# Kernel optimization log

Measured on AMD Instinct MI355X. Metric: run time of the kernel, lower is better.

## Reference

```python
import jax, jax.numpy as jnp
import numpy as np

L2_LAMDA = 0.001
RECONS_LAMDA = 0.2
LB_TH = 0.01
B, N, D = 32, 2048, 256


def setup_inputs() -> dict:
    key = jax.random.key(0)
    k1, k2, k3, k4 = jax.random.split(key, 4)
    cur = jax.random.normal(k1, (B, N, D), jnp.float32)
    pre = jax.random.normal(k2, (B, N, D), jnp.float32)
    lim_r = float(np.sqrt(6.0 / (D + D)))  # xavier_uniform bound
    r_proj = jax.random.uniform(k3, (D, D), jnp.float32, -lim_r, lim_r)
    lim_i = float(np.sqrt(6.0 / (N + N)))
    incidence_m = jax.random.uniform(k4, (N, N), jnp.float32, -lim_i, lim_i)
    return {"cur": cur, "pre": pre, "r_proj": r_proj, "incidence_m": incidence_m}


def reference(cur, pre, r_proj, incidence_m):
    # torch forward detaches cur/pre
    cur = jax.lax.stop_gradient(cur)
    pre = jax.lax.stop_gradient(pre)
    # clamp(min=lb_th) then zero where not (> lb_th)  ==  keep original where > lb_th else 0
    W = jnp.where(incidence_m > LB_TH, incidence_m, 0.0)          # (N, N)
    proj = jnp.einsum('bnd,de->bne', cur, r_proj)                 # (B, N, D)
    neigh = jnp.einsum('nm,bmd->bnd', W, pre)                     # (B, N, D)
    recon_err = jnp.sqrt(jnp.sum((proj - neigh) ** 2, axis=-1))   # (B, N)
    # torch: max(sum(abs(row[None,:]), dim=0)) == max-abs of the masked row
    l1 = jnp.max(jnp.abs(W), axis=1)                              # (N,)
    l2 = jnp.sqrt(jnp.sum(W ** 2, axis=1))                        # (N,)
    per_node = recon_err * RECONS_LAMDA + l1[None, :] + L2_LAMDA * l2[None, :]
    loss = jnp.sum(per_node, axis=1, keepdims=True)               # (B, 1)
    return loss, incidence_m
```

## Files before the change

kernel.cpp:

```cpp
#include <hip/hip_runtime.h>


typedef __attribute__((ext_vector_type(8))) short bf16x8;
typedef __attribute__((ext_vector_type(8))) unsigned short ushort8;
typedef __attribute__((ext_vector_type(16))) float f32x16;

__device__ __forceinline__ unsigned short f2bf(float f) {
    union { float f; unsigned u; } x; x.f = f;
    unsigned r = x.u + 0x7fffu + ((x.u >> 16) & 1u);
    return (unsigned short)(r >> 16);
}

#define GLL16(g, l)                                                         \
    __builtin_amdgcn_global_load_lds(                                       \
        (const __attribute__((address_space(1))) void*)(g),                 \
        (__attribute__((address_space(3))) void*)(l), 16, 0, 0)

__device__ __forceinline__ void transpose_64x64(
    const float* __restrict__ src, unsigned short* __restrict__ dst,
    int R, int C, int r0, int c0, unsigned short* __restrict__ tile) {
    const int t = threadIdx.x;
    const int fr = t >> 4, fc = (t & 15) * 4;
#pragma unroll
    for (int it = 0; it < 4; ++it) {
        int m = fr + it * 16;
        float4 v = *(const float4*)(src + (size_t)(r0 + m) * C + c0 + fc);
        tile[(fc + 0) * 68 + m] = f2bf(v.x);
        tile[(fc + 1) * 68 + m] = f2bf(v.y);
        tile[(fc + 2) * 68 + m] = f2bf(v.z);
        tile[(fc + 3) * 68 + m] = f2bf(v.w);
    }
    __syncthreads();
    const int d = t >> 2, m0 = (t & 3) * 16;
    unsigned short v[16];
#pragma unroll
    for (int j = 0; j < 4; ++j)
        *(ushort4*)(v + j * 4) = *(const ushort4*)(tile + d * 68 + m0 + j * 4);
    unsigned short* dp = dst + (size_t)(c0 + d) * R + r0 + m0;
    ushort8 p0, p1;
#pragma unroll
    for (int j = 0; j < 8; ++j) { p0[j] = v[j]; p1[j] = v[8 + j]; }
    *(ushort8*)(dp) = p0;
    *(ushort8*)(dp + 8) = p1;
}

__global__ __launch_bounds__(256) void prep_all(
    const float* __restrict__ inc, float* __restrict__ out_inc,
    unsigned short* __restrict__ Wneg, float* __restrict__ crow,
    const float* __restrict__ pre, unsigned short* __restrict__ preT,
    const float* __restrict__ r_proj, unsigned short* __restrict__ rprojT) {
    __shared__ unsigned short tile[64 * 68];
    __shared__ float smax[4], ssum[4];
    const int bid = blockIdx.x;
    const int t = threadIdx.x;

    if (bid < 2048) {
        const int row = bid;
        const float4* src = (const float4*)(inc + (size_t)row * 2048);
        float4* dst = (float4*)(out_inc + (size_t)row * 2048);
        ushort4* wp = (ushort4*)(Wneg + (size_t)row * 2048);
        float lmax = 0.f, ss = 0.f;
#pragma unroll
        for (int it = 0; it < 2; ++it) {
            int i = it * 256 + t;
            float4 v = src[i];
            dst[i] = v;
            float w0 = v.x > 0.01f ? v.x : 0.f;
            float w1 = v.y > 0.01f ? v.y : 0.f;
            float w2 = v.z > 0.01f ? v.z : 0.f;
            float w3 = v.w > 0.01f ? v.w : 0.f;
            ushort4 p;
            p.x = f2bf(-w0); p.y = f2bf(-w1); p.z = f2bf(-w2); p.w = f2bf(-w3);
            wp[i] = p;
            lmax = fmaxf(lmax, fmaxf(fmaxf(w0, w1), fmaxf(w2, w3)));
            ss += w0 * w0 + w1 * w1 + w2 * w2 + w3 * w3;
        }
#pragma unroll
        for (int off = 32; off; off >>= 1) {
            lmax = fmaxf(lmax, __shfl_down(lmax, off));
            ss += __shfl_down(ss, off);
        }
        int wv = t >> 6, ln = t & 63;
        if (ln == 0) { smax[wv] = lmax; ssum[wv] = ss; }
        __syncthreads();
        if (t == 0) {
            float m = fmaxf(fmaxf(smax[0], smax[1]), fmaxf(smax[2], smax[3]));
            float s = ssum[0] + ssum[1] + ssum[2] + ssum[3];
            crow[row] = m + 0.001f * sqrtf(s);
        }
    } else if (bid < 6144) {
        const int tt = bid - 2048;
        const int b = tt >> 7;
        const int mt = (tt & 127) >> 2;
        const int dt = tt & 3;
        transpose_64x64(pre + (size_t)b * 524288, preT + (size_t)b * 524288,
                        2048, 256, mt * 64, dt * 64, tile);
    } else {
        const int tt = bid - 6144;
        transpose_64x64(r_proj, rprojT, 256, 256, (tt >> 2) * 64, (tt & 3) * 64,
                        tile);
    }
}

__global__ __launch_bounds__(256, 2) void gemm_diff(
    const unsigned short* __restrict__ Wneg,
    const float* __restrict__ cur,
    const unsigned short* __restrict__ preT,
    const unsigned short* __restrict__ rprojT,
    float* __restrict__ Ssq)
{
    const int n0 = blockIdx.x * 128;
    const int b  = blockIdx.y;

    __shared__ unsigned short Al[128 * 64];
    __shared__ unsigned short Bl[256 * 64];
    __shared__ float ssq[128];

    const int tid  = threadIdx.x;
    const int w    = tid >> 6;
    const int lane = tid & 63;
    const int l32  = lane & 31;
    const int half = lane >> 5;
    const int wm   = w >> 1, wn = w & 1;

    if (tid < 128) ssq[tid] = 0.f;

    f32x16 acc[2][4] = {};

    const float*          curB = cur  + (size_t)b * 2048 * 256;
    const unsigned short* preB = preT + (size_t)b * 256 * 2048;

    const int grow  = lane >> 3;
    const int gbyte = ((lane & 7) ^ grow) * 16;
    const int sw    = (l32 & 7) * 8;

    for (int kt = 0; kt < 36; ++kt) {
        __syncthreads();
        if (kt < 32) {
            const int k0 = kt * 64;
            const unsigned short* ab = Wneg + (size_t)n0 * 2048 + k0;
#pragma unroll
            for (int j = 0; j < 4; ++j) {
                const int row = w * 32 + j * 8 + grow;
                GLL16((const char*)(ab + (size_t)row * 2048) + gbyte,
                      (char*)Al + w * 4096 + j * 1024);
            }
            const unsigned short* bb = preB + k0;
#pragma unroll
            for (int j = 0; j < 8; ++j) {
                const int row = w * 64 + j * 8 + grow;
                GLL16((const char*)(bb + (size_t)row * 2048) + gbyte,
                      (char*)Bl + w * 8192 + j * 1024);
            }
        } else {
            const int kk = kt * 64 - 2048;
            const int r16 = tid >> 4, k4 = tid & 15;
#pragma unroll
            for (int i = 0; i < 8; ++i) {
                const int row = r16 + i * 16;
                float4 v = *(const float4*)(curB + (size_t)(n0 + row) * 256 + kk + k4 * 4);
                ushort4 p;
                p.x = f2bf(v.x); p.y = f2bf(v.y); p.z = f2bf(v.z); p.w = f2bf(v.w);
                const int pos = ((k4 >> 1) ^ (row & 7)) * 8 + (k4 & 1) * 4;
                *(ushort4*)(Al + row * 64 + pos) = p;
            }
            const unsigned short* bb = rprojT + kk;
#pragma unroll
            for (int j = 0; j < 8; ++j) {
                const int row = w * 64 + j * 8 + grow;
                GLL16((const char*)(bb + (size_t)row * 256) + gbyte,
                      (char*)Bl + w * 8192 + j * 1024);
            }
        }
        __syncthreads();

#pragma unroll
        for (int ks = 0; ks < 4; ++ks) {
            const int ck = (ks * 2 + half) * 8;
            bf16x8 af[2], bfr[4];
#pragma unroll
            for (int mi = 0; mi < 2; ++mi)
                af[mi] = *(const bf16x8*)(Al + (wm * 64 + mi * 32 + l32) * 64 +
                                          (ck ^ sw));
#pragma unroll
            for (int ni = 0; ni < 4; ++ni)
                bfr[ni] = *(const bf16x8*)(Bl + (wn * 128 + ni * 32 + l32) * 64 +
                                           (ck ^ sw));
#pragma unroll
            for (int mi = 0; mi < 2; ++mi)
#pragma unroll
                for (int ni = 0; ni < 4; ++ni)
                    acc[mi][ni] = __builtin_amdgcn_mfma_f32_32x32x16_bf16(
                        af[mi], bfr[ni], acc[mi][ni], 0, 0, 0);
        }
    }
    __syncthreads();

#pragma unroll
    for (int mi = 0; mi < 2; ++mi)
#pragma unroll
        for (int reg = 0; reg < 16; ++reg) {
            float s = 0.f;
#pragma unroll
            for (int ni = 0; ni < 4; ++ni) {
                float v = acc[mi][ni][reg];
                s += v * v;
            }
            s += __shfl_xor(s, 1);
            s += __shfl_xor(s, 2);
            s += __shfl_xor(s, 4);
            s += __shfl_xor(s, 8);
            s += __shfl_xor(s, 16);
            if (l32 == 0) {
                const int row = (reg & 3) + 8 * (reg >> 2) + 4 * half;
                atomicAdd(&ssq[wm * 64 + mi * 32 + row], s);
            }
        }
    __syncthreads();
    if (tid < 128)
        Ssq[(size_t)b * 2048 + n0 + tid] = sqrtf(ssq[tid]);
}

__global__ void finalize(const float* __restrict__ Ssq,
                         const float* __restrict__ crow,
                         float* __restrict__ out) {
    const int b = blockIdx.x;
    float s1 = 0.f, s2 = 0.f;
    for (int i = threadIdx.x; i < 2048; i += 256) {
        s1 += Ssq[(size_t)b * 2048 + i];
        s2 += crow[i];
    }
#pragma unroll
    for (int off = 32; off; off >>= 1) {
        s1 += __shfl_down(s1, off);
        s2 += __shfl_down(s2, off);
    }
    __shared__ float sm1[4], sm2[4];
    int wv = threadIdx.x >> 6, ln = threadIdx.x & 63;
    if (ln == 0) { sm1[wv] = s1; sm2[wv] = s2; }
    __syncthreads();
    if (threadIdx.x == 0)
        out[b] = 0.2f * (sm1[0] + sm1[1] + sm1[2] + sm1[3])
               + (sm2[0] + sm2[1] + sm2[2] + sm2[3]);
}

extern "C" void kernel_launch(void* const* d_in, const int* in_sizes, int n_in,
                              void* d_out, int out_size, void* d_ws, size_t ws_size,
                              hipStream_t stream) {
    const float* cur    = (const float*)d_in[0];
    const float* pre    = (const float*)d_in[1];
    const float* r_proj = (const float*)d_in[2];
    const float* inc    = (const float*)d_in[3];
    float* out = (float*)d_out;

    char* ws = (char*)d_ws;
    unsigned short* Wneg   = (unsigned short*)(ws + 0);
    unsigned short* preT   = (unsigned short*)(ws + 8388608);
    unsigned short* rprojT = (unsigned short*)(ws + 41943040);
    float*          Sbuf   = (float*)(ws + 42074112);
    float*          crow   = (float*)(ws + 42336256);

    prep_all<<<6160, 256, 0, stream>>>(inc, out + 32, Wneg, crow,
                                       pre, preT, r_proj, rprojT);
    gemm_diff<<<dim3(16, 32), 256, 0, stream>>>(Wneg, cur, preT, rprojT, Sbuf);
    finalize<<<32, 256, 0, stream>>>(Sbuf, crow, out);
}
```

Before: 248.8 us.

## Enlarge GEMM tile to 256x256 with double-buffered LDS and phased prefetch pipeline

The fused diff GEMM moves from 128x256 tiles with 4 waves to 256x256 tiles with 8 waves (512 threads). The main K loop over W·pre now uses double-buffered LDS with global_load_lds prefetches interleaved across quarter-tile MFMA phases, fine-grained vmcnt waits, barriers and s_setprio around MFMA bursts. The goal is to hide global load latency and halve redundant B-tile traffic per output. In exchange it uses much more LDS (128KB+), which limits occupancy to one block per CU, and the grid shrinks to 256 blocks.

```diff
diff --git a/kernel.cpp b/kernel.cpp
--- a/kernel.cpp
+++ b/kernel.cpp
@@ -102,107 +102,162 @@
     }
 }
 
-__global__ __launch_bounds__(256, 2) void gemm_diff(
+__global__ __launch_bounds__(512, 2) void gemm_diff(
     const unsigned short* __restrict__ Wneg,
     const float* __restrict__ cur,
     const unsigned short* __restrict__ preT,
     const unsigned short* __restrict__ rprojT,
     float* __restrict__ Ssq)
 {
-    const int n0 = blockIdx.x * 128;
+    const int n0 = blockIdx.x * 256;
     const int b  = blockIdx.y;
 
-    __shared__ unsigned short Al[128 * 64];
-    __shared__ unsigned short Bl[256 * 64];
-    __shared__ float ssq[128];
-
-    const int tid  = threadIdx.x;
-    const int w    = tid >> 6;
-    const int lane = tid & 63;
-    const int l32  = lane & 31;
-    const int half = lane >> 5;
-    const int wm   = w >> 1, wn = w & 1;
-
-    if (tid < 128) ssq[tid] = 0.f;
-
-    f32x16 acc[2][4] = {};
-
-    const float*          curB = cur  + (size_t)b * 2048 * 256;
-    const unsigned short* preB = preT + (size_t)b * 256 * 2048;
-
+    __shared__ unsigned short Al[2][256 * 64];
+    __shared__ unsigned short Bl[2][256 * 64];
+    __shared__ float ssq[256];
+
+    const int tid   = threadIdx.x;
+    const int w     = tid >> 6;
+    const int lane  = tid & 63;
+    const int l32   = lane & 31;
+    const int half  = lane >> 5;
+    const int wm128 = (w >> 2) * 128;
+    const int wn64  = (w & 3) * 64;
+    const int w8    = w * 8;
     const int grow  = lane >> 3;
     const int gbyte = ((lane & 7) ^ grow) * 16;
     const int sw    = (l32 & 7) * 8;
 
-    for (int kt = 0; kt < 36; ++kt) {
+    if (tid < 256) ssq[tid] = 0.f;
+
+    f32x16 acc[4][2] = {};
+
+    const float*          curB = cur  + (size_t)b * 2048 * 256;
+    const unsigned short* preB = preT + (size_t)b * 256 * 2048;
+    const unsigned short* An   = Wneg + (size_t)n0 * 2048;
+
+#define STAGE_A(AP, qa, K0)                                                    \
+    {                                                                          \
+        _Pragma("unroll") for (int pass = 0; pass < 2; ++pass) {               \
+            const int rowb = (qa) * 64 + pass * 128 + w8;                      \
+            GLL16((const char*)(An + (size_t)(rowb + grow) * 2048 + (K0)) + gbyte, \
+                  (char*)(AP) + rowb * 128);                                   \
+        }                                                                      \
+    }
+#define STAGE_B(BP, u, K0)                                                     \
+    {                                                                          \
+        _Pragma("unroll") for (int pass = 0; pass < 2; ++pass) {               \
+            const int rowb = (u) * 128 + pass * 64 + w8;                       \
+            GLL16((const char*)(preB + (size_t)(rowb + grow) * 2048 + (K0)) + gbyte, \
+                  (char*)(BP) + rowb * 128);                                   \
+        }                                                                      \
+    }
+
+    STAGE_A(Al[0], 0, 0);
+    STAGE_B(Bl[0], 0, 0);
+    STAGE_B(Bl[0], 1, 0);
+    STAGE_A(Al[0], 1, 0);
+    STAGE_A(Al[1], 0, 64);
+    asm volatile("s_waitcnt vmcnt(2)" ::: "memory");
+    asm volatile("s_barrier" ::: "memory");
+
+    bf16x8 bfr[2][2];
+
+#define LOADB(BP, kh)                                                          \
+    _Pragma("unroll") for (int ni = 0; ni < 2; ++ni)                           \
+    _Pragma("unroll") for (int ksl = 0; ksl < 2; ++ksl)                        \
+        bfr[ni][ksl] = *(const bf16x8*)((BP) + (wn64 + ni * 32 + l32) * 64 +   \
+                           (((((kh) * 2 + ksl) * 2 + half) * 8) ^ sw));
+
+#define PHASE(AP, qa, kh, STAGES, VMW)                                         \
+    {                                                                          \
+        bf16x8 af[2][2];                                                       \
+        _Pragma("unroll") for (int mi = 0; mi < 2; ++mi)                       \
+        _Pragma("unroll") for (int ksl = 0; ksl < 2; ++ksl)                    \
+            af[mi][ksl] = *(const bf16x8*)((AP) +                              \
+                (wm128 + (qa) * 64 + mi * 32 + l32) * 64 +                     \
+                (((((kh) * 2 + ksl) * 2 + half) * 8) ^ sw));                   \
+        STAGES                                                                 \
+        VMW                                                                    \
+        asm volatile("s_barrier" ::: "memory");                                \
+        __builtin_amdgcn_s_setprio(1);                                         \
+        _Pragma("unroll") for (int mi = 0; mi < 2; ++mi)                       \
+        _Pragma("unroll") for (int ni = 0; ni < 2; ++ni)                       \
+        _Pragma("unroll") for (int ksl = 0; ksl < 2; ++ksl)                    \
+            acc[(qa) * 2 + mi][ni] = __builtin_amdgcn_mfma_f32_32x32x16_bf16(  \
+                af[mi][ksl], bfr[ni][ksl], acc[(qa) * 2 + mi][ni], 0, 0, 0);   \
+        __builtin_amdgcn_s_setprio(0);                                         \
+        asm volatile("s_barrier" ::: "memory");                                \
+    }
+
+    for (int j = 0; j < 16; ++j) {
+        const int k1 = (2 * j + 1) * 64;
+        const int k2 = (2 * j + 2) * 64;
+        const int k3 = (2 * j + 3) * 64;
+        const bool s2 = (2 * j + 2) < 32;
+        const bool s3 = (2 * j + 3) < 32;
+
+        LOADB(Bl[0], 0);
+        PHASE(Al[0], 0, 0, { STAGE_A(Al[1], 1, k1); STAGE_B(Bl[1], 0, k1); }, {})
+        PHASE(Al[0], 1, 0, { STAGE_B(Bl[1], 1, k1); }, {})
+        LOADB(Bl[0], 1);
+        PHASE(Al[0], 0, 1, {}, {})
+        PHASE(Al[0], 1, 1, { if (s2) STAGE_A(Al[0], 0, k2); },
+              { if (j == 15) { asm volatile("s_waitcnt vmcnt(0)" ::: "memory"); }
+                else         { asm volatile("s_waitcnt vmcnt(2)" ::: "memory"); } })
+        LOADB(Bl[1], 0);
+        PHASE(Al[1], 0, 0, { if (s2) { STAGE_A(Al[0], 1, k2); STAGE_B(Bl[0], 0, k2); } }, {})
+        PHASE(Al[1], 1, 0, { if (s2) STAGE_B(Bl[0], 1, k2); }, {})
+        LOADB(Bl[1], 1);
+        PHASE(Al[1], 0, 1, {}, {})
+        PHASE(Al[1], 1, 1, { if (s3) STAGE_A(Al[1], 0, k3); },
+              { if (j < 15) { asm volatile("s_waitcnt vmcnt(2)" ::: "memory"); } })
+    }
+
+    for (int kt = 32; kt < 36; ++kt) {
         __syncthreads();
-        if (kt < 32) {
-            const int k0 = kt * 64;
-            const unsigned short* ab = Wneg + (size_t)n0 * 2048 + k0;
-#pragma unroll
-            for (int j = 0; j < 4; ++j) {
-                const int row = w * 32 + j * 8 + grow;
-                GLL16((const char*)(ab + (size_t)row * 2048) + gbyte,
-                      (char*)Al + w * 4096 + j * 1024);
-            }
-            const unsigned short* bb = preB + k0;
-#pragma unroll
-            for (int j = 0; j < 8; ++j) {
-                const int row = w * 64 + j * 8 + grow;
-                GLL16((const char*)(bb + (size_t)row * 2048) + gbyte,
-                      (char*)Bl + w * 8192 + j * 1024);
-            }
-        } else {
-            const int kk = kt * 64 - 2048;
-            const int r16 = tid >> 4, k4 = tid & 15;
-#pragma unroll
-            for (int i = 0; i < 8; ++i) {
-                const int row = r16 + i * 16;
-                float4 v = *(const float4*)(curB + (size_t)(n0 + row) * 256 + kk + k4 * 4);
-                ushort4 p;
-                p.x = f2bf(v.x); p.y = f2bf(v.y); p.z = f2bf(v.z); p.w = f2bf(v.w);
-                const int pos = ((k4 >> 1) ^ (row & 7)) * 8 + (k4 & 1) * 4;
-                *(ushort4*)(Al + row * 64 + pos) = p;
-            }
-            const unsigned short* bb = rprojT + kk;
-#pragma unroll
-            for (int j = 0; j < 8; ++j) {
-                const int row = w * 64 + j * 8 + grow;
-                GLL16((const char*)(bb + (size_t)row * 256) + gbyte,
-                      (char*)Bl + w * 8192 + j * 1024);
-            }
+        const int kk = (kt - 32) * 64;
+        const int r16 = tid >> 4, k4 = tid & 15;
+#pragma unroll
+        for (int i = 0; i < 8; ++i) {
+            const int row = r16 + i * 32;
+            float4 v = *(const float4*)(curB + (size_t)(n0 + row) * 256 + kk + k4 * 4);
+            ushort4 p;
+            p.x = f2bf(v.x); p.y = f2bf(v.y); p.z = f2bf(v.z); p.w = f2bf(v.w);
+            const int pos = ((k4 >> 1) ^ (row & 7)) * 8 + (k4 & 1) * 4;
+            *(ushort4*)(&Al[0][row * 64 + pos]) = p;
+        }
+#pragma unroll
+        for (int pass = 0; pass < 4; ++pass) {
+            const int rowb = pass * 64 + w8;
+            GLL16((const char*)(rprojT + (size_t)(rowb + grow) * 256 + kk) + gbyte,
+                  (char*)&Bl[0][0] + rowb * 128);
         }
         __syncthreads();
-
 #pragma unroll
         for (int ks = 0; ks < 4; ++ks) {
             const int ck = (ks * 2 + half) * 8;
-            bf16x8 af[2], bfr[4];
-#pragma unroll
-            for (int mi = 0; mi < 2; ++mi)
-                af[mi] = *(const bf16x8*)(Al + (wm * 64 + mi * 32 + l32) * 64 +
-                                          (ck ^ sw));
-#pragma unroll
-            for (int ni = 0; ni < 4; ++ni)
-                bfr[ni] = *(const bf16x8*)(Bl + (wn * 128 + ni * 32 + l32) * 64 +
-                                           (ck ^ sw));
-#pragma unroll
-            for (int mi = 0; mi < 2; ++mi)
-#pragma unroll
-                for (int ni = 0; ni < 4; ++ni)
+#pragma unroll
+            for (int mi = 0; mi < 4; ++mi) {
+                bf16x8 af = *(const bf16x8*)(&Al[0][(wm128 + mi * 32 + l32) * 64 + (ck ^ sw)]);
+#pragma unroll
+                for (int ni = 0; ni < 2; ++ni) {
+                    bf16x8 bv = *(const bf16x8*)(&Bl[0][(wn64 + ni * 32 + l32) * 64 + (ck ^ sw)]);
                     acc[mi][ni] = __builtin_amdgcn_mfma_f32_32x32x16_bf16(
-                        af[mi], bfr[ni], acc[mi][ni], 0, 0, 0);
+                        af, bv, acc[mi][ni], 0, 0, 0);
+                }
+            }
         }
     }
     __syncthreads();
 
 #pragma unroll
-    for (int mi = 0; mi < 2; ++mi)
+    for (int mi = 0; mi < 4; ++mi)
 #pragma unroll
         for (int reg = 0; reg < 16; ++reg) {
             float s = 0.f;
 #pragma unroll
-            for (int ni = 0; ni < 4; ++ni) {
+            for (int ni = 0; ni < 2; ++ni) {
                 float v = acc[mi][ni][reg];
                 s += v * v;
             }
@@ -213,11 +268,11 @@
             s += __shfl_xor(s, 16);
             if (l32 == 0) {
                 const int row = (reg & 3) + 8 * (reg >> 2) + 4 * half;
-                atomicAdd(&ssq[wm * 64 + mi * 32 + row], s);
+                atomicAdd(&ssq[wm128 + mi * 32 + row], s);
             }
         }
     __syncthreads();
-    if (tid < 128)
+    if (tid < 256)
         Ssq[(size_t)b * 2048 + n0 + tid] = sqrtf(ssq[tid]);
 }
 
@@ -262,6 +317,6 @@
 
     prep_all<<<6160, 256, 0, stream>>>(inc, out + 32, Wneg, crow,
                                        pre, preT, r_proj, rprojT);
-    gemm_diff<<<dim3(16, 32), 256, 0, stream>>>(Wneg, cur, preT, rprojT, Sbuf);
+    gemm_diff<<<dim3(8, 32), 512, 0, stream>>>(Wneg, cur, preT, rprojT, Sbuf);
     finalize<<<32, 256, 0, stream>>>(Sbuf, crow, out);
 }
```

Result: no change. 248.8 us (+0.0%).

## Double-buffer GEMM LDS tiles with 1024-thread 256x256 blocks and split prep kernels

Applied to the files above, without the earlier changes.

The GEMM kernel moves from 128x256 tiles with 4 waves to 256x256 tiles with 16 waves per block. Its main K loop now double-buffers the A/B LDS tiles, issuing async global-to-LDS loads for the next tile while MFMAs run on the current one, which is meant to hide load latency and halve the number of blocks re-reading preT. The prep kernel is split into separate incidence and transpose kernels. The trade-offs are a grid of only 256 blocks, each with 128KB of LDS so one block per CU, and an extra kernel launch.

```diff
diff --git a/kernel.cpp b/kernel.cpp
--- a/kernel.cpp
+++ b/kernel.cpp
@@ -44,155 +44,164 @@
     *(ushort8*)(dp + 8) = p1;
 }
 
-__global__ __launch_bounds__(256) void prep_all(
+__global__ __launch_bounds__(256) void prep_inc(
     const float* __restrict__ inc, float* __restrict__ out_inc,
-    unsigned short* __restrict__ Wneg, float* __restrict__ crow,
+    unsigned short* __restrict__ Wneg, float* __restrict__ crow) {
+    __shared__ float smax[4], ssum[4];
+    const int row = blockIdx.x;
+    const int t = threadIdx.x;
+    const float4* src = (const float4*)(inc + (size_t)row * 2048);
+    float4* dst = (float4*)(out_inc + (size_t)row * 2048);
+    ushort4* wp = (ushort4*)(Wneg + (size_t)row * 2048);
+    float lmax = 0.f, ss = 0.f;
+#pragma unroll
+    for (int it = 0; it < 2; ++it) {
+        int i = it * 256 + t;
+        float4 v = src[i];
+        dst[i] = v;
+        float w0 = v.x > 0.01f ? v.x : 0.f;
+        float w1 = v.y > 0.01f ? v.y : 0.f;
+        float w2 = v.z > 0.01f ? v.z : 0.f;
+        float w3 = v.w > 0.01f ? v.w : 0.f;
+        ushort4 p;
+        p.x = f2bf(-w0); p.y = f2bf(-w1); p.z = f2bf(-w2); p.w = f2bf(-w3);
+        wp[i] = p;
+        lmax = fmaxf(lmax, fmaxf(fmaxf(w0, w1), fmaxf(w2, w3)));
+        ss += w0 * w0 + w1 * w1 + w2 * w2 + w3 * w3;
+    }
+#pragma unroll
+    for (int off = 32; off; off >>= 1) {
+        lmax = fmaxf(lmax, __shfl_down(lmax, off));
+        ss += __shfl_down(ss, off);
+    }
+    int wv = t >> 6, ln = t & 63;
+    if (ln == 0) { smax[wv] = lmax; ssum[wv] = ss; }
+    __syncthreads();
+    if (t == 0) {
+        float m = fmaxf(fmaxf(smax[0], smax[1]), fmaxf(smax[2], smax[3]));
+        float s = ssum[0] + ssum[1] + ssum[2] + ssum[3];
+        crow[row] = m + 0.001f * sqrtf(s);
+    }
+}
+
+__global__ __launch_bounds__(256) void prep_tr(
     const float* __restrict__ pre, unsigned short* __restrict__ preT,
     const float* __restrict__ r_proj, unsigned short* __restrict__ rprojT) {
     __shared__ unsigned short tile[64 * 68];
-    __shared__ float smax[4], ssum[4];
     const int bid = blockIdx.x;
-    const int t = threadIdx.x;
-
-    if (bid < 2048) {
-        const int row = bid;
-        const float4* src = (const float4*)(inc + (size_t)row * 2048);
-        float4* dst = (float4*)(out_inc + (size_t)row * 2048);
-        ushort4* wp = (ushort4*)(Wneg + (size_t)row * 2048);
-        float lmax = 0.f, ss = 0.f;
-#pragma unroll
-        for (int it = 0; it < 2; ++it) {
-            int i = it * 256 + t;
-            float4 v = src[i];
-            dst[i] = v;
-            float w0 = v.x > 0.01f ? v.x : 0.f;
-            float w1 = v.y > 0.01f ? v.y : 0.f;
-            float w2 = v.z > 0.01f ? v.z : 0.f;
-            float w3 = v.w > 0.01f ? v.w : 0.f;
-            ushort4 p;
-            p.x = f2bf(-w0); p.y = f2bf(-w1); p.z = f2bf(-w2); p.w = f2bf(-w3);
-            wp[i] = p;
-            lmax = fmaxf(lmax, fmaxf(fmaxf(w0, w1), fmaxf(w2, w3)));
-            ss += w0 * w0 + w1 * w1 + w2 * w2 + w3 * w3;
-        }
-#pragma unroll
-        for (int off = 32; off; off >>= 1) {
-            lmax = fmaxf(lmax, __shfl_down(lmax, off));
-            ss += __shfl_down(ss, off);
-        }
-        int wv = t >> 6, ln = t & 63;
-        if (ln == 0) { smax[wv] = lmax; ssum[wv] = ss; }
-        __syncthreads();
-        if (t == 0) {
-            float m = fmaxf(fmaxf(smax[0], smax[1]), fmaxf(smax[2], smax[3]));
-            float s = ssum[0] + ssum[1] + ssum[2] + ssum[3];
-            crow[row] = m + 0.001f * sqrtf(s);
-        }
-    } else if (bid < 6144) {
-        const int tt = bid - 2048;
-        const int b = tt >> 7;
-        const int mt = (tt & 127) >> 2;
-        const int dt = tt & 3;
+    if (bid < 4096) {
+        const int b = bid >> 7;
+        const int mt = (bid & 127) >> 2;
+        const int dt = bid & 3;
         transpose_64x64(pre + (size_t)b * 524288, preT + (size_t)b * 524288,
                         2048, 256, mt * 64, dt * 64, tile);
     } else {
-        const int tt = bid - 6144;
+        const int tt = bid - 4096;
         transpose_64x64(r_proj, rprojT, 256, 256, (tt >> 2) * 64, (tt & 3) * 64,
                         tile);
     }
 }
 
-__global__ __launch_bounds__(256, 2) void gemm_diff(
+__global__ __launch_bounds__(1024) void gemm_diff(
     const unsigned short* __restrict__ Wneg,
     const float* __restrict__ cur,
     const unsigned short* __restrict__ preT,
     const unsigned short* __restrict__ rprojT,
     float* __restrict__ Ssq)
 {
-    const int n0 = blockIdx.x * 128;
+    const int n0 = blockIdx.x * 256;
     const int b  = blockIdx.y;
 
-    __shared__ unsigned short Al[128 * 64];
-    __shared__ unsigned short Bl[256 * 64];
-    __shared__ float ssq[128];
+    __shared__ unsigned short Al[2 * 256 * 64];
+    __shared__ unsigned short Bl[2 * 256 * 64];
+    __shared__ float ssq[256];
 
     const int tid  = threadIdx.x;
     const int w    = tid >> 6;
     const int lane = tid & 63;
     const int l32  = lane & 31;
     const int half = lane >> 5;
-    const int wm   = w >> 1, wn = w & 1;
-
-    if (tid < 128) ssq[tid] = 0.f;
-
-    f32x16 acc[2][4] = {};
-
-    const float*          curB = cur  + (size_t)b * 2048 * 256;
-    const unsigned short* preB = preT + (size_t)b * 256 * 2048;
-
+    const int wm   = w >> 2;
+    const int wn   = w & 3;
+    const int w8   = w * 8;
     const int grow  = lane >> 3;
     const int gbyte = ((lane & 7) ^ grow) * 16;
     const int sw    = (l32 & 7) * 8;
 
-    for (int kt = 0; kt < 36; ++kt) {
+    if (tid < 256) ssq[tid] = 0.f;
+
+    f32x16 acc[2][2] = {};
+
+    const float*          curB = cur  + (size_t)b * 2048 * 256;
+    const unsigned short* preB = preT + (size_t)b * 256 * 2048;
+    const unsigned short* An   = Wneg + (size_t)n0 * 2048;
+
+#define STAGE_TILE(AP, BP, K0)                                                 \
+    {                                                                          \
+        _Pragma("unroll") for (int pass = 0; pass < 2; ++pass) {               \
+            const int rowb = pass * 128 + w8;                                  \
+            GLL16((const char*)(An + (size_t)(rowb + grow) * 2048 + (K0)) + gbyte, \
+                  (char*)(AP) + rowb * 128);                                   \
+        }                                                                      \
+        _Pragma("unroll") for (int pass = 0; pass < 2; ++pass) {               \
+            const int rowb = pass * 128 + w8;                                  \
+            GLL16((const char*)(preB + (size_t)(rowb + grow) * 2048 + (K0)) + gbyte, \
+                  (char*)(BP) + rowb * 128);                                   \
+        }                                                                      \
+    }
+
+#define KS_LOOP(Ac, Bc)                                                        \
+    _Pragma("unroll") for (int ks = 0; ks < 4; ++ks) {                         \
+        const int ck = (ks * 2 + half) * 8;                                    \
+        bf16x8 af[2], bfr[2];                                                  \
+        _Pragma("unroll") for (int mi = 0; mi < 2; ++mi)                       \
+            af[mi] = *(const bf16x8*)((Ac) + (wm * 64 + mi * 32 + l32) * 64 +  \
+                                      (ck ^ sw));                              \
+        _Pragma("unroll") for (int ni = 0; ni < 2; ++ni)                       \
+            bfr[ni] = *(const bf16x8*)((Bc) + (wn * 64 + ni * 32 + l32) * 64 + \
+                                       (ck ^ sw));                             \
+        _Pragma("unroll") for (int mi = 0; mi < 2; ++mi)                       \
+        _Pragma("unroll") for (int ni = 0; ni < 2; ++ni)                       \
+            acc[mi][ni] = __builtin_amdgcn_mfma_f32_32x32x16_bf16(             \
+                af[mi], bfr[ni], acc[mi][ni], 0, 0, 0);                        \
+    }
+
+    STAGE_TILE(Al, Bl, 0);
+
+    for (int t = 0; t < 32; ++t) {
+        unsigned short* Ac = Al + (t & 1) * 16384;
+        unsigned short* Bc = Bl + (t & 1) * 16384;
+        unsigned short* Anx = Al + ((t & 1) ^ 1) * 16384;
+        unsigned short* Bnx = Bl + ((t & 1) ^ 1) * 16384;
+
+        asm volatile("s_waitcnt vmcnt(0)" ::: "memory");
+        asm volatile("s_barrier" ::: "memory");
+        if (t < 31) { STAGE_TILE(Anx, Bnx, (t + 1) * 64); }
+        KS_LOOP(Ac, Bc)
+    }
+
+    for (int kt = 32; kt < 36; ++kt) {
         __syncthreads();
-        if (kt < 32) {
-            const int k0 = kt * 64;
-            const unsigned short* ab = Wneg + (size_t)n0 * 2048 + k0;
-#pragma unroll
-            for (int j = 0; j < 4; ++j) {
-                const int row = w * 32 + j * 8 + grow;
-                GLL16((const char*)(ab + (size_t)row * 2048) + gbyte,
-                      (char*)Al + w * 4096 + j * 1024);
-            }
-            const unsigned short* bb = preB + k0;
-#pragma unroll
-            for (int j = 0; j < 8; ++j) {
-                const int row = w * 64 + j * 8 + grow;
-                GLL16((const char*)(bb + (size_t)row * 2048) + gbyte,
-                      (char*)Bl + w * 8192 + j * 1024);
-            }
-        } else {
-            const int kk = kt * 64 - 2048;
-            const int r16 = tid >> 4, k4 = tid & 15;
-#pragma unroll
-            for (int i = 0; i < 8; ++i) {
-                const int row = r16 + i * 16;
-                float4 v = *(const float4*)(curB + (size_t)(n0 + row) * 256 + kk + k4 * 4);
-                ushort4 p;
-                p.x = f2bf(v.x); p.y = f2bf(v.y); p.z = f2bf(v.z); p.w = f2bf(v.w);
-                const int pos = ((k4 >> 1) ^ (row & 7)) * 8 + (k4 & 1) * 4;
-                *(ushort4*)(Al + row * 64 + pos) = p;
-            }
-            const unsigned short* bb = rprojT + kk;
-#pragma unroll
-            for (int j = 0; j < 8; ++j) {
-                const int row = w * 64 + j * 8 + grow;
-                GLL16((const char*)(bb + (size_t)row * 256) + gbyte,
-                      (char*)Bl + w * 8192 + j * 1024);
-            }
+        const int kk = (kt - 32) * 64;
+        const int row = tid >> 2;
+        const int q   = tid & 3;
+#pragma unroll
+        for (int i = 0; i < 4; ++i) {
+            const int k4 = q * 4 + i;
+            float4 v = *(const float4*)(curB + (size_t)(n0 + row) * 256 + kk + k4 * 4);
+            ushort4 p;
+            p.x = f2bf(v.x); p.y = f2bf(v.y); p.z = f2bf(v.z); p.w = f2bf(v.w);
+            const int pos = ((k4 >> 1) ^ (row & 7)) * 8 + (k4 & 1) * 4;
+            *(ushort4*)(Al + row * 64 + pos) = p;
+        }
+#pragma unroll
+        for (int pass = 0; pass < 2; ++pass) {
+            const int rowb = pass * 128 + w8;
+            GLL16((const char*)(rprojT + (size_t)(rowb + grow) * 256 + kk) + gbyte,
+                  (char*)Bl + rowb * 128);
         }
         __syncthreads();
-
-#pragma unroll
-        for (int ks = 0; ks < 4; ++ks) {
-            const int ck = (ks * 2 + half) * 8;
-            bf16x8 af[2], bfr[4];
-#pragma unroll
-            for (int mi = 0; mi < 2; ++mi)
-                af[mi] = *(const bf16x8*)(Al + (wm * 64 + mi * 32 + l32) * 64 +
-                                          (ck ^ sw));
-#pragma unroll
-            for (int ni = 0; ni < 4; ++ni)
-                bfr[ni] = *(const bf16x8*)(Bl + (wn * 128 + ni * 32 + l32) * 64 +
-                                           (ck ^ sw));
-#pragma unroll
-            for (int mi = 0; mi < 2; ++mi)
-#pragma unroll
-                for (int ni = 0; ni < 4; ++ni)
-                    acc[mi][ni] = __builtin_amdgcn_mfma_f32_32x32x16_bf16(
-                        af[mi], bfr[ni], acc[mi][ni], 0, 0, 0);
-        }
+        KS_LOOP(Al, Bl)
     }
     __syncthreads();
 
@@ -202,7 +211,7 @@
         for (int reg = 0; reg < 16; ++reg) {
             float s = 0.f;
 #pragma unroll
-            for (int ni = 0; ni < 4; ++ni) {
+            for (int ni = 0; ni < 2; ++ni) {
                 float v = acc[mi][ni][reg];
                 s += v * v;
             }
@@ -212,12 +221,13 @@
             s += __shfl_xor(s, 8);
             s += __shfl_xor(s, 16);
             if (l32 == 0) {
-                const int row = (reg & 3) + 8 * (reg >> 2) + 4 * half;
-                atomicAdd(&ssq[wm * 64 + mi * 32 + row], s);
+                const int row = wm * 64 + mi * 32 +
+                                (reg & 3) + 8 * (reg >> 2) + 4 * half;
+                atomicAdd(&ssq[row], s);
             }
         }
     __syncthreads();
-    if (tid < 128)
+    if (tid < 256)
         Ssq[(size_t)b * 2048 + n0 + tid] = sqrtf(ssq[tid]);
 }
 
@@ -260,8 +270,8 @@
     float*          Sbuf   = (float*)(ws + 42074112);
     float*          crow   = (float*)(ws + 42336256);
 
-    prep_all<<<6160, 256, 0, stream>>>(inc, out + 32, Wneg, crow,
-                                       pre, preT, r_proj, rprojT);
-    gemm_diff<<<dim3(16, 32), 256, 0, stream>>>(Wneg, cur, preT, rprojT, Sbuf);
+    prep_inc<<<2048, 256, 0, stream>>>(inc, out + 32, Wneg, crow);
+    prep_tr<<<4112, 256, 0, stream>>>(pre, preT, r_proj, rprojT);
+    gemm_diff<<<dim3(8, 32), 1024, 0, stream>>>(Wneg, cur, preT, rprojT, Sbuf);
     finalize<<<32, 256, 0, stream>>>(Sbuf, crow, out);
 }
```

After: 254.6 us. 2.3% more time.
